# Optimization experiments

Hardware: AMD Instinct MI355X
Metric: run time of the kernel (lower is better)

## Reference

```python
import jax, jax.numpy as jnp
import numpy as np

B, T, D, H = 2, 4096, 512, 8
DH = D // H  # dim_head = 64


def setup_inputs() -> dict:
    key = jax.random.key(0)
    ks = jax.random.split(key, 10)
    s = 1.0 / np.sqrt(D)
    x = jax.random.normal(ks[0], (B, T, D), dtype=jnp.float32)
    Wq = jax.random.uniform(ks[1], (D, D), jnp.float32, -s, s)
    Wk = jax.random.uniform(ks[2], (D, D), jnp.float32, -s, s)
    Wv = jax.random.uniform(ks[3], (D, D), jnp.float32, -s, s)
    Wo = jax.random.uniform(ks[4], (D, D), jnp.float32, -s, s)
    bq = jnp.zeros((D,), jnp.float32)
    bk = jnp.zeros((D,), jnp.float32)
    bv = jnp.zeros((D,), jnp.float32)
    bo = jnp.zeros((D,), jnp.float32)
    mask = jax.random.randint(ks[5], (1, 1, T, T), 0, 2).astype(bool)
    return {"x": x, "Wq": Wq, "bq": bq, "Wk": Wk, "bk": bk,
            "Wv": Wv, "bv": bv, "Wo": Wo, "bo": bo, "mask": mask}


def reference(x, Wq, bq, Wk, bk, Wv, bv, Wo, bo, mask):
    # QKV projections (self-attention: Q=K=V=x)
    def split_heads(t):
        return t.reshape(B, T, H, DH).transpose(0, 2, 1, 3)  # (B,H,T,DH)
    Q = split_heads(x @ Wq + bq)
    K = split_heads(x @ Wk + bk)
    V = split_heads(x @ Wv + bv)
    # scaled dot-product attention with additive mask penalty (as in source)
    scores = jnp.einsum('bhqd,bhkd->bhqk', Q, K) / np.sqrt(DH)
    scores = scores + (~mask).astype(scores.dtype) * (-1e9)
    att_w = jax.nn.softmax(scores, axis=-1)
    O = jnp.einsum('bhqk,bhkd->bhqd', att_w, V)
    O = O.transpose(0, 2, 1, 3).reshape(B, T, D)
    return O @ Wo + bo
```

## Files before the change

### kernel.cpp

```cpp
#include <hip/hip_runtime.h>
#include <stdint.h>

#define B_ 2
#define T_ 4096
#define D_ 512
#define H_ 8
#define DH_ 64

typedef __bf16 bf16;
typedef __bf16 bf16x4_t __attribute__((ext_vector_type(4)));
typedef __bf16 bf16x8_t __attribute__((ext_vector_type(8)));
typedef float f32x4 __attribute__((ext_vector_type(4)));
typedef short short4_t __attribute__((ext_vector_type(4)));
typedef uint32_t u32;

static constexpr float QSCALE = 0.18033688011112042f;

__device__ __forceinline__ void async16(void* lds, const void* g) {
  __builtin_amdgcn_global_load_lds(
      (const __attribute__((address_space(1))) void*)g,
      (__attribute__((address_space(3))) void*)lds, 16, 0, 0);
}

__global__ __launch_bounds__(256) void prep_kernel(
    const float* __restrict__ x,
    const float* __restrict__ Wq, const float* __restrict__ Wk,
    const float* __restrict__ Wv, const float* __restrict__ Wo,
    const void* __restrict__ maskp,
    bf16* __restrict__ xb, bf16* __restrict__ WTall, bf16* __restrict__ WoT,
    u32* __restrict__ bmask)
{
  int bid = blockIdx.x;
  int tid = threadIdx.x;
  if (bid < 4096) {
    int idx = bid * 256 + tid;
    const float4* xf = (const float4*)x;
    float4 v = xf[idx];
    bf16x4_t o;
    o[0] = (bf16)v.x; o[1] = (bf16)v.y; o[2] = (bf16)v.z; o[3] = (bf16)v.w;
    ((bf16x4_t*)xb)[idx] = o;
  } else if (bid < 8192) {
    int gid = (bid - 4096) * 256 + tid;
    int sel = gid >> 18;
    int idx = gid & 262143;
    int n = idx >> 9, k = idx & 511;
    if (sel < 3) {
      const float* W = (sel == 0) ? Wq : (sel == 1) ? Wk : Wv;
      float v = W[k * 512 + n];
      if (sel == 0) v *= QSCALE;
      WTall[gid] = (bf16)v;
    } else {
      WoT[idx] = (bf16)Wo[k * 512 + n];
    }
  } else {
    int wid = (bid - 8192) * 256 + tid;
    const uint8_t* m8 = (const uint8_t*)maskp;
    bool u8mode = (__ballot(m8[4 * (tid & 63) + 1] != 0) != 0ull);
    int row = wid >> 7, wcol = wid & 127;
    size_t off = (size_t)row * 4096 + (size_t)wcol * 32;
    u32 w = 0;
    if (u8mode) {
      const uint4* p = (const uint4*)(m8 + off);
      uint4 a = p[0], b = p[1];
      u32 ws[8] = {a.x, a.y, a.z, a.w, b.x, b.y, b.z, b.w};
      #pragma unroll
      for (int j = 0; j < 32; ++j)
        if ((ws[j >> 2] >> ((j & 3) * 8)) & 0xffu) w |= (1u << j);
    } else {
      const uint4* p = (const uint4*)((const u32*)maskp + off);
      #pragma unroll
      for (int q = 0; q < 8; ++q) {
        uint4 a = p[q];
        if (a.x) w |= 1u << (q * 4 + 0);
        if (a.y) w |= 1u << (q * 4 + 1);
        if (a.z) w |= 1u << (q * 4 + 2);
        if (a.w) w |= 1u << (q * 4 + 3);
      }
    }
    bmask[((size_t)(row >> 6) * 64 + (wcol >> 1)) * 128 + (row & 63) * 2 + (wcol & 1)] = w;
  }
}

__global__ __launch_bounds__(256) void qkv_kernel(
    const bf16* __restrict__ xb, const bf16* __restrict__ WTall,
    const float* __restrict__ bq, const float* __restrict__ bk,
    const float* __restrict__ bv,
    bf16* __restrict__ Qb, bf16* __restrict__ Kb, bf16* __restrict__ Vtb)
{
  __shared__ char smem[16384];
  char* smX = smem;
  char* smW = smem + 8192;
  int tid = threadIdx.x;
  int lane = tid & 63, wave = tid >> 6;
  int lo = lane & 15, quad = lane >> 4;
  int wr = wave >> 1, wc = wave & 1;
  int bm = blockIdx.x * 64;
  int bn = blockIdx.y * 64;
  int sel = bn >> 9;
  f32x4 acc[2][2] = {};
  for (int kc = 0; kc < 8; ++kc) {
    __syncthreads();
    for (int s = tid; s < 512; s += 256) {
      int row = s >> 3, slot = s & 7;
      int cg = slot ^ (row & 7) ^ ((row >> 3) & 1);
      async16(smX + s * 16, xb + (size_t)(bm + row) * 512 + kc * 64 + cg * 8);
      async16(smW + s * 16, WTall + (size_t)(bn + row) * 512 + kc * 64 + cg * 8);
    }
    __syncthreads();
    #pragma unroll
    for (int ks = 0; ks < 2; ++ks) {
      bf16x8_t a[2], b[2];
      #pragma unroll
      for (int mt = 0; mt < 2; ++mt) {
        int row = wr * 32 + mt * 16 + lo;
        int ch = (ks * 4 + quad) ^ (row & 7) ^ ((row >> 3) & 1);
        a[mt] = *(const bf16x8_t*)(smX + row * 128 + ch * 16);
      }
      #pragma unroll
      for (int nt = 0; nt < 2; ++nt) {
        int row = wc * 32 + nt * 16 + lo;
        int ch = (ks * 4 + quad) ^ (row & 7) ^ ((row >> 3) & 1);
        b[nt] = *(const bf16x8_t*)(smW + row * 128 + ch * 16);
      }
      if (sel < 2) {
        #pragma unroll
        for (int mt = 0; mt < 2; ++mt)
          #pragma unroll
          for (int nt = 0; nt < 2; ++nt)
            acc[mt][nt] = __builtin_amdgcn_mfma_f32_16x16x32_bf16(
                b[nt], a[mt], acc[mt][nt], 0, 0, 0);
      } else {
        #pragma unroll
        for (int mt = 0; mt < 2; ++mt)
          #pragma unroll
          for (int nt = 0; nt < 2; ++nt)
            acc[mt][nt] = __builtin_amdgcn_mfma_f32_16x16x32_bf16(
                a[mt], b[nt], acc[mt][nt], 0, 0, 0);
      }
    }
  }
  int b_ = bm >> 12;
  if (sel < 2) {
    const float* bias = (sel == 0) ? bq : bk;
    bf16* base = (sel == 0) ? Qb : Kb;
    #pragma unroll
    for (int mt = 0; mt < 2; ++mt) {
      int t = (bm & 4095) + wr * 32 + mt * 16 + lo;
      #pragma unroll
      for (int nt = 0; nt < 2; ++nt) {
        int n0 = (bn + wc * 32 + nt * 16 + quad * 4) & 511;
        int h = n0 >> 6, dh0 = n0 & 63;
        bf16x4_t v;
        #pragma unroll
        for (int r = 0; r < 4; ++r) {
          float bs = bias[n0 + r];
          if (sel == 0) bs *= QSCALE;
          v[r] = (bf16)(acc[mt][nt][r] + bs);
        }
        *(bf16x4_t*)(base + (size_t)(b_ * H_ + h) * T_ * DH_ +
                     (size_t)t * 64 + dh0) = v;
      }
    }
  } else {
    #pragma unroll
    for (int nt = 0; nt < 2; ++nt) {
      int n0 = (bn + wc * 32 + nt * 16 + lo) & 511;
      int h = n0 >> 6, dh = n0 & 63;
      float bs = bv[n0];
      #pragma unroll
      for (int mt = 0; mt < 2; ++mt) {
        int t0 = (bm & 4095) + wr * 32 + mt * 16 + quad * 4;
        bf16x4_t v;
        #pragma unroll
        for (int r = 0; r < 4; ++r) v[r] = (bf16)(acc[mt][nt][r] + bs);
        *(bf16x4_t*)(Vtb + ((size_t)(b_ * H_ + h) * DH_ + dh) * T_ + t0) = v;
      }
    }
  }
}

__global__ __launch_bounds__(256, 4) void attn_kernel(
    const bf16* __restrict__ Qb, const bf16* __restrict__ Kb,
    const bf16* __restrict__ Vtb, const u32* __restrict__ bm2,
    bf16* __restrict__ Obuf)
{
  __shared__ char smem[17408];
  char* smK = smem;
  char* smV = smem + 8192;
  u32* smM = (u32*)(smem + 16384);
  float* smLa = (float*)(smem + 16896);
  float* smLb = (float*)(smem + 17152);
  int tid = threadIdx.x;
  int lane = tid & 63, wave = tid >> 6;
  int lo = lane & 15, quad = lane >> 4;
  int qh = wave & 1, kh = wave >> 1;
  int blk = blockIdx.x;
  int bh = blk & 15;
  int qt64 = blk >> 4;
  int qbase = qt64 * 64;

  const bf16* Kg = Kb + (size_t)bh * T_ * DH_;
  const bf16* Vg = Vtb + (size_t)bh * DH_ * T_;
  const u32* mg = bm2 + (size_t)qt64 * 8192;

  const bf16* Qg = Qb + ((size_t)bh * T_ + qbase + qh * 32) * DH_;
  bf16x8_t qf[2][2];
  #pragma unroll
  for (int qt = 0; qt < 2; ++qt)
    #pragma unroll
    for (int ks = 0; ks < 2; ++ks)
      qf[qt][ks] = *(const bf16x8_t*)(Qg + (qt * 16 + lo) * 64 + ks * 32 + quad * 8);

  short one = (lo == 0) ? (short)0x3F80 : (short)0;
  short4_t ones = {one, one, one, one};

  f32x4 O[2][4] = {};
  f32x4 Ol[2] = {};

  for (int kc = 0; kc < 64; ++kc) {
    __syncthreads();
    #pragma unroll
    for (int i = 0; i < 2; ++i) {
      int s = tid + i * 256;
      int row = s >> 3, slot = s & 7;
      int cg = slot ^ (row & 7) ^ ((row >> 3) & 1);
      async16(smK + s * 16, Kg + (size_t)(kc * 64 + row) * 64 + cg * 8);
      async16(smV + s * 16, Vg + (size_t)row * T_ + kc * 64 + cg * 8);
    }
    if (tid < 32) async16((char*)smM + tid * 16, mg + kc * 128 + tid * 4);
    __syncthreads();
    f32x4 St[2][2] = {};
    #pragma unroll
    for (int ks = 0; ks < 2; ++ks)
      #pragma unroll
      for (int kt = 0; kt < 2; ++kt) {
        int krow = kh * 32 + kt * 16 + lo;
        int ch = (ks * 4 + quad) ^ (krow & 7) ^ ((krow >> 3) & 1);
        bf16x8_t kf = *(const bf16x8_t*)(smK + krow * 128 + ch * 16);
        #pragma unroll
        for (int qt = 0; qt < 2; ++qt)
          St[kt][qt] = __builtin_amdgcn_mfma_f32_16x16x32_bf16(
              kf, qf[qt][ks], St[kt][qt], 0, 0, 0);
      }
    short4_t pf[2][2];
    #pragma unroll
    for (int qt = 0; qt < 2; ++qt) {
      u32 w = smM[(qh * 32 + qt * 16 + lo) * 2 + kh] >> (quad * 4);
      #pragma unroll
      for (int kt = 0; kt < 2; ++kt) {
        bf16x4_t t;
        #pragma unroll
        for (int r = 0; r < 4; ++r) {
          int mb = ((int)(w << (31 - (kt * 16 + r)))) >> 31;
          u32 pe = __builtin_bit_cast(u32, __builtin_amdgcn_exp2f(St[kt][qt][r]));
          t[r] = (bf16)__builtin_bit_cast(float, pe & (u32)mb);
        }
        pf[qt][kt] = __builtin_bit_cast(short4_t, t);
      }
    }
    #pragma unroll
    for (int kt = 0; kt < 2; ++kt)
      #pragma unroll
      for (int qt = 0; qt < 2; ++qt)
        Ol[qt] = __builtin_amdgcn_mfma_f32_16x16x16bf16_1k(
            pf[qt][kt], ones, Ol[qt], 0, 0, 0);
    #pragma unroll
    for (int dt = 0; dt < 4; ++dt) {
      int d = dt * 16 + lo;
      #pragma unroll
      for (int kt = 0; kt < 2; ++kt) {
        int c0 = kh * 4 + kt * 2 + (quad >> 1);
        int c = c0 ^ (d & 7) ^ ((d >> 3) & 1);
        short4_t vf = *(const short4_t*)(
            smV + d * 128 + c * 16 + ((quad & 1) << 3));
        #pragma unroll
        for (int qt = 0; qt < 2; ++qt)
          O[qt][dt] = __builtin_amdgcn_mfma_f32_16x16x16bf16_1k(
              pf[qt][kt], vf, O[qt][dt], 0, 0, 0);
      }
    }
  }
  __syncthreads();
  float* smO = (float*)smem;
  if (lo == 0) {
    float* dst = (kh == 0) ? smLa : smLb;
    #pragma unroll
    for (int qt = 0; qt < 2; ++qt)
      #pragma unroll
      for (int r = 0; r < 4; ++r)
        dst[qh * 32 + qt * 16 + quad * 4 + r] = Ol[qt][r];
  }
  if (kh == 1) {
    #pragma unroll
    for (int qt = 0; qt < 2; ++qt)
      #pragma unroll
      for (int dt = 0; dt < 4; ++dt)
        #pragma unroll
        for (int r = 0; r < 4; ++r)
          smO[(qh * 32 + qt * 16 + quad * 4 + r) * 64 + dt * 16 + lo] = O[qt][dt][r];
  }
  __syncthreads();
  if (kh == 0) {
    bf16* Og = Obuf + ((size_t)bh * T_ + qbase + qh * 32) * DH_;
    #pragma unroll
    for (int qt = 0; qt < 2; ++qt) {
      #pragma unroll
      for (int r = 0; r < 4; ++r) {
        int rl = qt * 16 + quad * 4 + r;
        float inv = 1.0f / (smLa[qh * 32 + rl] + smLb[qh * 32 + rl]);
        #pragma unroll
        for (int dt = 0; dt < 4; ++dt) {
          float o = (O[qt][dt][r] + smO[(qh * 32 + rl) * 64 + dt * 16 + lo]) * inv;
          Og[(size_t)rl * 64 + dt * 16 + lo] = (bf16)o;
        }
      }
    }
  }
}

__global__ __launch_bounds__(256) void proj_kernel(
    const bf16* __restrict__ Obuf, const bf16* __restrict__ WoT,
    const float* __restrict__ bo, float* __restrict__ out)
{
  __shared__ char smem[16384];
  char* smA = smem;
  char* smW = smem + 8192;
  int tid = threadIdx.x;
  int lane = tid & 63, wave = tid >> 6;
  int lo = lane & 15, quad = lane >> 4;
  int wr = wave >> 1, wc = wave & 1;
  int bm = blockIdx.x * 64;
  int bn = blockIdx.y * 64;
  int b_ = bm >> 12, trow = bm & 4095;
  f32x4 acc[2][2] = {};
  for (int kc = 0; kc < 8; ++kc) {
    __syncthreads();
    const bf16* Ag = Obuf + ((size_t)(b_ * H_ + kc) * T_ + trow) * DH_;
    for (int s = tid; s < 512; s += 256) {
      int row = s >> 3, slot = s & 7;
      int cg = slot ^ (row & 7) ^ ((row >> 3) & 1);
      async16(smA + s * 16, Ag + row * 64 + cg * 8);
      async16(smW + s * 16, WoT + (size_t)(bn + row) * 512 + kc * 64 + cg * 8);
    }
    __syncthreads();
    #pragma unroll
    for (int ks = 0; ks < 2; ++ks) {
      bf16x8_t a[2], b[2];
      #pragma unroll
      for (int mt = 0; mt < 2; ++mt) {
        int row = wr * 32 + mt * 16 + lo;
        int ch = (ks * 4 + quad) ^ (row & 7) ^ ((row >> 3) & 1);
        a[mt] = *(const bf16x8_t*)(smA + row * 128 + ch * 16);
      }
      #pragma unroll
      for (int nt = 0; nt < 2; ++nt) {
        int row = wc * 32 + nt * 16 + lo;
        int ch = (ks * 4 + quad) ^ (row & 7) ^ ((row >> 3) & 1);
        b[nt] = *(const bf16x8_t*)(smW + row * 128 + ch * 16);
      }
      #pragma unroll
      for (int mt = 0; mt < 2; ++mt)
        #pragma unroll
        for (int nt = 0; nt < 2; ++nt)
          acc[mt][nt] = __builtin_amdgcn_mfma_f32_16x16x32_bf16(
              b[nt], a[mt], acc[mt][nt], 0, 0, 0);
    }
  }
  #pragma unroll
  for (int mt = 0; mt < 2; ++mt) {
    int t = bm + wr * 32 + mt * 16 + lo;
    #pragma unroll
    for (int nt = 0; nt < 2; ++nt) {
      int c0 = bn + wc * 32 + nt * 16 + quad * 4;
      float4 v;
      v.x = acc[mt][nt][0] + bo[c0 + 0];
      v.y = acc[mt][nt][1] + bo[c0 + 1];
      v.z = acc[mt][nt][2] + bo[c0 + 2];
      v.w = acc[mt][nt][3] + bo[c0 + 3];
      *(float4*)(out + (size_t)t * 512 + c0) = v;
    }
  }
}

extern "C" void kernel_launch(void* const* d_in, const int* in_sizes, int n_in,
                              void* d_out, int out_size, void* d_ws, size_t ws_size,
                              hipStream_t stream) {
  const float* x  = (const float*)d_in[0];
  const float* Wq = (const float*)d_in[1];
  const float* bq = (const float*)d_in[2];
  const float* Wk = (const float*)d_in[3];
  const float* bk = (const float*)d_in[4];
  const float* Wv = (const float*)d_in[5];
  const float* bv = (const float*)d_in[6];
  const float* Wo = (const float*)d_in[7];
  const float* bo = (const float*)d_in[8];
  const void* maskp = d_in[9];
  float* out = (float*)d_out;

  char* w = (char*)d_ws;
  bf16* xb    = (bf16*)(w);
  bf16* WTall = (bf16*)(w + 8388608);
  bf16* WoT   = (bf16*)(w + 9961472);
  bf16* Qb    = (bf16*)(w + 10485760);
  bf16* Kb    = (bf16*)(w + 18874368);
  bf16* Vtb   = (bf16*)(w + 27262976);
  bf16* Obuf  = (bf16*)(w + 35651584);
  u32*  bmask = (u32*)(w + 44040192);

  prep_kernel<<<10240, 256, 0, stream>>>(x, Wq, Wk, Wv, Wo, maskp,
                                         xb, WTall, WoT, bmask);
  qkv_kernel<<<dim3(128, 24), 256, 0, stream>>>(xb, WTall, bq, bk, bv,
                                                Qb, Kb, Vtb);
  attn_kernel<<<1024, 256, 0, stream>>>(Qb, Kb, Vtb, bmask, Obuf);
  proj_kernel<<<dim3(128, 8), 256, 0, stream>>>(Obuf, WoT, bo, out);
}
```

Baseline: 275.0 us.

## Split attention key chunk across four waves with 32-query blocks

Each attention block now handles 32 queries instead of 64. All four waves share the same queries and each wave takes a 16-key slice of every 64-key chunk. The grid doubles to 2048 blocks, and the occupancy hint rises to 8 blocks per CU so more blocks can stay resident. Partial outputs and row sums from the four waves are combined through a tree reduction in padded LDS at the end. The trade-off is that each K/V tile is now loaded for half as many queries, doubling total K/V traffic, and the final reduction costs more.

```diff
diff --git a/kernel.cpp b/kernel.cpp
--- a/kernel.cpp
+++ b/kernel.cpp
@@ -179,7 +179,7 @@
   }
 }
 
-__global__ __launch_bounds__(256, 4) void attn_kernel(
+__global__ __launch_bounds__(256, 8) void attn_kernel(
     const bf16* __restrict__ Qb, const bf16* __restrict__ Kb,
     const bf16* __restrict__ Vtb, const u32* __restrict__ bm2,
     bf16* __restrict__ Obuf)
@@ -188,22 +188,20 @@
   char* smK = smem;
   char* smV = smem + 8192;
   u32* smM = (u32*)(smem + 16384);
-  float* smLa = (float*)(smem + 16896);
-  float* smLb = (float*)(smem + 17152);
+  float* smL = (float*)(smem + 16896);
   int tid = threadIdx.x;
-  int lane = tid & 63, wave = tid >> 6;
+  int lane = tid & 63, kh = tid >> 6;
   int lo = lane & 15, quad = lane >> 4;
-  int qh = wave & 1, kh = wave >> 1;
   int blk = blockIdx.x;
   int bh = blk & 15;
-  int qt64 = blk >> 4;
-  int qbase = qt64 * 64;
+  int qt32 = blk >> 4;
+  int qbase = qt32 * 32;
 
   const bf16* Kg = Kb + (size_t)bh * T_ * DH_;
   const bf16* Vg = Vtb + (size_t)bh * DH_ * T_;
-  const u32* mg = bm2 + (size_t)qt64 * 8192;
-
-  const bf16* Qg = Qb + ((size_t)bh * T_ + qbase + qh * 32) * DH_;
+  const u32* mg = bm2 + (size_t)(qt32 >> 1) * 8192 + (qt32 & 1) * 64;
+
+  const bf16* Qg = Qb + ((size_t)bh * T_ + qbase) * DH_;
   bf16x8_t qf[2][2];
   #pragma unroll
   for (int qt = 0; qt < 2; ++qt)
@@ -227,91 +225,102 @@
       async16(smK + s * 16, Kg + (size_t)(kc * 64 + row) * 64 + cg * 8);
       async16(smV + s * 16, Vg + (size_t)row * T_ + kc * 64 + cg * 8);
     }
-    if (tid < 32) async16((char*)smM + tid * 16, mg + kc * 128 + tid * 4);
-    __syncthreads();
-    f32x4 St[2][2] = {};
-    #pragma unroll
-    for (int ks = 0; ks < 2; ++ks)
-      #pragma unroll
-      for (int kt = 0; kt < 2; ++kt) {
-        int krow = kh * 32 + kt * 16 + lo;
-        int ch = (ks * 4 + quad) ^ (krow & 7) ^ ((krow >> 3) & 1);
-        bf16x8_t kf = *(const bf16x8_t*)(smK + krow * 128 + ch * 16);
-        #pragma unroll
-        for (int qt = 0; qt < 2; ++qt)
-          St[kt][qt] = __builtin_amdgcn_mfma_f32_16x16x32_bf16(
-              kf, qf[qt][ks], St[kt][qt], 0, 0, 0);
-      }
-    short4_t pf[2][2];
+    if (tid < 16) async16((char*)smM + tid * 16, mg + kc * 128 + tid * 4);
+    __syncthreads();
+    f32x4 St[2] = {};
+    #pragma unroll
+    for (int ks = 0; ks < 2; ++ks) {
+      int krow = kh * 16 + lo;
+      int ch = (ks * 4 + quad) ^ (krow & 7) ^ ((krow >> 3) & 1);
+      bf16x8_t kf = *(const bf16x8_t*)(smK + krow * 128 + ch * 16);
+      #pragma unroll
+      for (int qt = 0; qt < 2; ++qt)
+        St[qt] = __builtin_amdgcn_mfma_f32_16x16x32_bf16(
+            kf, qf[qt][ks], St[qt], 0, 0, 0);
+    }
+    short4_t pf[2];
     #pragma unroll
     for (int qt = 0; qt < 2; ++qt) {
-      u32 w = smM[(qh * 32 + qt * 16 + lo) * 2 + kh] >> (quad * 4);
-      #pragma unroll
-      for (int kt = 0; kt < 2; ++kt) {
-        bf16x4_t t;
-        #pragma unroll
-        for (int r = 0; r < 4; ++r) {
-          int mb = ((int)(w << (31 - (kt * 16 + r)))) >> 31;
-          u32 pe = __builtin_bit_cast(u32, __builtin_amdgcn_exp2f(St[kt][qt][r]));
-          t[r] = (bf16)__builtin_bit_cast(float, pe & (u32)mb);
-        }
-        pf[qt][kt] = __builtin_bit_cast(short4_t, t);
-      }
-    }
-    #pragma unroll
-    for (int kt = 0; kt < 2; ++kt)
-      #pragma unroll
-      for (int qt = 0; qt < 2; ++qt)
-        Ol[qt] = __builtin_amdgcn_mfma_f32_16x16x16bf16_1k(
-            pf[qt][kt], ones, Ol[qt], 0, 0, 0);
+      u32 w = smM[(qt * 16 + lo) * 2 + (kh >> 1)] >> ((kh & 1) * 16 + quad * 4);
+      bf16x4_t t;
+      #pragma unroll
+      for (int r = 0; r < 4; ++r) {
+        int mb = ((int)(w << (31 - r))) >> 31;
+        u32 pe = __builtin_bit_cast(u32, __builtin_amdgcn_exp2f(St[qt][r]));
+        t[r] = (bf16)__builtin_bit_cast(float, pe & (u32)mb);
+      }
+      pf[qt] = __builtin_bit_cast(short4_t, t);
+    }
+    #pragma unroll
+    for (int qt = 0; qt < 2; ++qt)
+      Ol[qt] = __builtin_amdgcn_mfma_f32_16x16x16bf16_1k(
+          pf[qt], ones, Ol[qt], 0, 0, 0);
     #pragma unroll
     for (int dt = 0; dt < 4; ++dt) {
       int d = dt * 16 + lo;
-      #pragma unroll
-      for (int kt = 0; kt < 2; ++kt) {
-        int c0 = kh * 4 + kt * 2 + (quad >> 1);
-        int c = c0 ^ (d & 7) ^ ((d >> 3) & 1);
-        short4_t vf = *(const short4_t*)(
-            smV + d * 128 + c * 16 + ((quad & 1) << 3));
-        #pragma unroll
-        for (int qt = 0; qt < 2; ++qt)
-          O[qt][dt] = __builtin_amdgcn_mfma_f32_16x16x16bf16_1k(
-              pf[qt][kt], vf, O[qt][dt], 0, 0, 0);
-      }
+      int c = (kh * 2 + (quad >> 1)) ^ (d & 7) ^ ((d >> 3) & 1);
+      short4_t vf = *(const short4_t*)(
+          smV + d * 128 + c * 16 + ((quad & 1) << 3));
+      #pragma unroll
+      for (int qt = 0; qt < 2; ++qt)
+        O[qt][dt] = __builtin_amdgcn_mfma_f32_16x16x16bf16_1k(
+            pf[qt], vf, O[qt][dt], 0, 0, 0);
     }
   }
   __syncthreads();
-  float* smO = (float*)smem;
+  float* bufA = (float*)smem;
+  float* bufB = (float*)(smem + 8320);
   if (lo == 0) {
-    float* dst = (kh == 0) ? smLa : smLb;
     #pragma unroll
     for (int qt = 0; qt < 2; ++qt)
       #pragma unroll
       for (int r = 0; r < 4; ++r)
-        dst[qh * 32 + qt * 16 + quad * 4 + r] = Ol[qt][r];
-  }
-  if (kh == 1) {
+        smL[kh * 32 + qt * 16 + quad * 4 + r] = Ol[qt][r];
+  }
+  if (kh & 1) {
+    float* buf = (kh == 1) ? bufA : bufB;
     #pragma unroll
     for (int qt = 0; qt < 2; ++qt)
       #pragma unroll
       for (int dt = 0; dt < 4; ++dt)
         #pragma unroll
         for (int r = 0; r < 4; ++r)
-          smO[(qh * 32 + qt * 16 + quad * 4 + r) * 64 + dt * 16 + lo] = O[qt][dt][r];
+          buf[(qt * 16 + quad * 4 + r) * 65 + dt * 16 + lo] = O[qt][dt][r];
+  }
+  __syncthreads();
+  if (!(kh & 1)) {
+    float* buf = (kh == 0) ? bufA : bufB;
+    #pragma unroll
+    for (int qt = 0; qt < 2; ++qt)
+      #pragma unroll
+      for (int dt = 0; dt < 4; ++dt)
+        #pragma unroll
+        for (int r = 0; r < 4; ++r)
+          O[qt][dt][r] += buf[(qt * 16 + quad * 4 + r) * 65 + dt * 16 + lo];
+  }
+  if (kh == 2) {
+    #pragma unroll
+    for (int qt = 0; qt < 2; ++qt)
+      #pragma unroll
+      for (int dt = 0; dt < 4; ++dt)
+        #pragma unroll
+        for (int r = 0; r < 4; ++r)
+          bufB[(qt * 16 + quad * 4 + r) * 65 + dt * 16 + lo] = O[qt][dt][r];
   }
   __syncthreads();
   if (kh == 0) {
-    bf16* Og = Obuf + ((size_t)bh * T_ + qbase + qh * 32) * DH_;
+    bf16* Og = Obuf + ((size_t)bh * T_ + qbase) * DH_;
     #pragma unroll
     for (int qt = 0; qt < 2; ++qt) {
       #pragma unroll
       for (int r = 0; r < 4; ++r) {
-        int rl = qt * 16 + quad * 4 + r;
-        float inv = 1.0f / (smLa[qh * 32 + rl] + smLb[qh * 32 + rl]);
+        int q = qt * 16 + quad * 4 + r;
+        float tot = (smL[q] + smL[32 + q]) + (smL[64 + q] + smL[96 + q]);
+        float inv = 1.0f / tot;
         #pragma unroll
         for (int dt = 0; dt < 4; ++dt) {
-          float o = (O[qt][dt][r] + smO[(qh * 32 + rl) * 64 + dt * 16 + lo]) * inv;
-          Og[(size_t)rl * 64 + dt * 16 + lo] = (bf16)o;
+          float o = (O[qt][dt][r] + bufB[q * 65 + dt * 16 + lo]) * inv;
+          Og[(size_t)q * 64 + dt * 16 + lo] = (bf16)o;
         }
       }
     }
@@ -411,6 +420,6 @@
                                          xb, WTall, WoT, bmask);
   qkv_kernel<<<dim3(128, 24), 256, 0, stream>>>(xb, WTall, bq, bk, bv,
                                                 Qb, Kb, Vtb);
-  attn_kernel<<<1024, 256, 0, stream>>>(Qb, Kb, Vtb, bmask, Obuf);
+  attn_kernel<<<2048, 256, 0, stream>>>(Qb, Kb, Vtb, bmask, Obuf);
   proj_kernel<<<dim3(128, 8), 256, 0, stream>>>(Obuf, WoT, bo, out);
 }
```

Result: slower. 718.5 us (+161.3%).
